# Optimization experiments

Measured on AMD Instinct MI355X. Metric: run time of the kernel, lower is better.

## Reference

```python
import jax, jax.numpy as jnp
import numpy as np

N, NC, D, K = 262144, 4096, 5, 4   # fine dof, coarse dof, nnz/row of A, interp points/row of P
W = 2.0 / 3.0                      # weighted-Jacobi weight
PRE, POST, COARSE = 3, 3, 10       # smoothing counts from the source


def setup_inputs() -> dict:
    key = jax.random.key(0)
    k1, k2, k3, k4, k5 = jax.random.split(key, 5)
    # A in ELL form: slot 0 is the diagonal, made strictly diagonally dominant.
    acols_off = jax.random.randint(k1, (N, D - 1), 0, N)
    A_cols = jnp.concatenate([jnp.arange(N)[:, None], acols_off], axis=1).astype(jnp.int32)
    off = -jax.random.uniform(k2, (N, D - 1), dtype=jnp.float32)          # negative off-diagonals (M-matrix-like)
    diag = 2.0 + jnp.sum(jnp.abs(off), axis=1)
    A_vals = jnp.concatenate([diag[:, None], off], axis=1)
    # P in ELL form: slot 0 maps fine node i -> coarse node i // (N//NC) so every coarse dof is covered.
    pcols_off = jax.random.randint(k3, (N, K - 1), 0, NC)
    P_cols = jnp.concatenate([(jnp.arange(N) // (N // NC))[:, None], pcols_off], axis=1).astype(jnp.int32)
    P_vals = jax.random.uniform(k4, (N, K), dtype=jnp.float32) * 0.5
    b = jax.random.normal(k5, (N,), dtype=jnp.float32)
    x = jnp.zeros((N,), dtype=jnp.float32)
    return {"b": b, "x": x, "A_vals": A_vals, "P_vals": P_vals,
            "A_cols": A_cols, "P_cols": P_cols, "num": 2}


def _spmv(vals, cols, x):
    # ELL SpMV: y[i] = sum_d vals[i,d] * x[cols[i,d]]
    return jnp.sum(vals * x[cols], axis=1)


def _jacobi_ell(vals, cols, diag, b, x, n):
    def step(xc, _):
        return xc + W * (b - _spmv(vals, cols, xc)) / diag, None
    x, _ = jax.lax.scan(step, x, None, length=n)
    return x


def _rap(A_vals, A_cols, P_vals, P_cols):
    # A_c = P^T A P, assembled densely on the coarse level via one big scatter-add.
    Pj_vals = P_vals[A_cols]                                   # [N,D,K]
    Pj_cols = P_cols[A_cols]                                   # [N,D,K]
    vals = (P_vals[:, None, :, None] * A_vals[:, :, None, None]
            * Pj_vals[:, :, None, :])                          # [N,D,K,K]
    a_idx = jnp.broadcast_to(P_cols[:, None, :, None].astype(jnp.int32), (N, D, K, K))
    b_idx = jnp.broadcast_to(Pj_cols[:, :, None, :].astype(jnp.int32), (N, D, K, K))
    flat = (a_idx * NC + b_idx).reshape(-1)
    Ac = jax.ops.segment_sum(vals.reshape(-1), flat, num_segments=NC * NC)
    return Ac.reshape(NC, NC)


def reference(b, x, A_vals, P_vals, A_cols, P_cols, num):
    diag_f = A_vals[:, 0]                      # fine-level diagonal (slot 0)
    Ac = _rap(A_vals, A_cols, P_vals, P_cols)  # coarse operator R A P
    diag_c = jnp.diag(Ac)

    def coarse_solve(bc):
        def step(xc, _):
            return xc + W * (bc - Ac @ xc) / diag_c, None
        xc, _ = jax.lax.scan(step, jnp.zeros((NC,), bc.dtype), None, length=COARSE)
        return xc

    for _ in range(num):                       # mg.Iterate, `num` V-cycles
        x = _jacobi_ell(A_vals, A_cols, diag_f, b, x, PRE)          # pre-smooth
        r = b - _spmv(A_vals, A_cols, x)                            # residual
        bc = jax.ops.segment_sum((P_vals * r[:, None]).reshape(-1),  # restrict: R r = P^T r
                                 P_cols.reshape(-1), num_segments=NC)
        xc = coarse_solve(bc)                                       # coarse Jacobi solve
        x = x + jnp.sum(P_vals * xc[P_cols], axis=1)                # prolongate correction
        x = _jacobi_ell(A_vals, A_cols, diag_f, b, x, POST)         # post-smooth
    return x
```

## Files before the change

### kernel.cpp

```cpp
#include <hip/hip_runtime.h>
#include <hip/hip_fp16.h>

#define NN 262144
#define NCC 4096
#define DD 5
#define PRE_IT 3
#define POST_IT 3
#define COARSE_IT 10
#define WJ ((float)(2.0/3.0))
#define NBLK 256
#define BAR_SLOT_U32 768
#define BAR_SLOTS 40
#define POISON 0xAAAAAAAAu
#define BASE_SUM 0x55555540u

typedef unsigned long long u64;

__device__ __forceinline__ unsigned pack_ch(unsigned col, float v) {
  return col | ((unsigned)__half_as_ushort(__float2half(v)) << 16);
}
__device__ __forceinline__ float unpack_h(unsigned w) {
  return __half2float(__ushort_as_half((unsigned short)(w >> 16)));
}

__device__ __forceinline__ float ldA(const float* p) {
  return __hip_atomic_load(p, __ATOMIC_RELAXED, __HIP_MEMORY_SCOPE_AGENT);
}
__device__ __forceinline__ void stA(float* p, float v) {
  __hip_atomic_store(p, v, __ATOMIC_RELAXED, __HIP_MEMORY_SCOPE_AGENT);
}
__device__ __forceinline__ unsigned ldAu(const unsigned* p) {
  return __hip_atomic_load(p, __ATOMIC_RELAXED, __HIP_MEMORY_SCOPE_AGENT);
}
__device__ __forceinline__ void stAu(unsigned* p, unsigned v) {
  __hip_atomic_store(p, v, __ATOMIC_RELAXED, __HIP_MEMORY_SCOPE_AGENT);
}
__device__ __forceinline__ u64 ldA64(const u64* p) {
  return __hip_atomic_load(p, __ATOMIC_RELAXED, __HIP_MEMORY_SCOPE_AGENT);
}
__device__ __forceinline__ void stA64(u64* p, u64 v) {
  __hip_atomic_store(p, v, __ATOMIC_RELAXED, __HIP_MEMORY_SCOPE_AGENT);
}

__device__ __forceinline__ void gbar(unsigned* bar, int& bs, int* sflag) {
  __syncthreads();
  if (threadIdx.x == 0) {
    unsigned* slot  = bar + bs * BAR_SLOT_U32;
    unsigned* line  = slot + ((blockIdx.x & 31) << 4);
    unsigned* flags = slot + 512;
    unsigned r = __hip_atomic_fetch_add(line, 1u, __ATOMIC_RELAXED,
                                        __HIP_MEMORY_SCOPE_AGENT);
    if ((blockIdx.x & 31) == 0 && r == POISON + 7u) {
      for (;;) {
        unsigned s = 0;
#pragma unroll
        for (int i = 0; i < 32; ++i) s += ldAu(slot + (i << 4));
        if (s - BASE_SUM >= 256u) break;
        __builtin_amdgcn_s_sleep(1);
      }
#pragma unroll
      for (int f = 0; f < 16; ++f) stAu(flags + (f << 4), POISON + 1u);
    }
    const unsigned* fl = flags + ((blockIdx.x & 15) << 4);
    while (ldAu(fl) == POISON) __builtin_amdgcn_s_sleep(1);
    __hip_atomic_store(sflag, bs + 1, __ATOMIC_RELAXED, __HIP_MEMORY_SCOPE_WORKGROUP);
  } else if ((threadIdx.x & 63) == 0) {
    while (__hip_atomic_load(sflag, __ATOMIC_RELAXED, __HIP_MEMORY_SCOPE_WORKGROUP) <= bs)
      __builtin_amdgcn_s_sleep(1);
  }
  ++bs;
}

__global__ __launch_bounds__(1024, 4) void k_all(
    const float* __restrict__ b, const float* __restrict__ x_in,
    const float* __restrict__ A_vals, const float* __restrict__ P_vals,
    const int* __restrict__ A_cols, const int* __restrict__ P_cols,
    const int* __restrict__ num_p,
    unsigned* histG, unsigned* offsG, u64* pairs8,
    unsigned* Y, unsigned* tot,
    unsigned* bar, float* partials, float* x2,
    float* xcA, float* xcB, float* out) {
  extern __shared__ char smem[];
  __shared__ float wdiag[16];
  __shared__ float bcl[16];
  __shared__ unsigned soffs[17];
  __shared__ int sflag;

  const int tid = threadIdx.x;
  const int blk = blockIdx.x;
  const int g = (blk << 10) + tid;
  int bs = 0;
  if (tid == 0) sflag = 0;

  const int4* pc4 = (const int4*)P_cols;
  const float4* pv4 = (const float4*)P_vals;
  unsigned* base_t = histG;

  const int4 pcg = pc4[g];
  const float4 pvg = pv4[g];
  const bool strx = (pcg.x == (g >> 6));
  u64 yreg0, yreg1, yreg2, yreg3, yreg4, yreg5, yreg6, yreg7, yreg8, yreg9;

  {
    unsigned* s1 = (unsigned*)smem;
    unsigned* s2 = s1 + NCC;
    unsigned* s3 = s2 + NCC;
    unsigned* sv = s3 + NCC;

    for (int q = tid; q < NCC; q += 1024) s1[q] = 0u;
    __syncthreads();
    {
      int ac[DD]; float av[DD];
#pragma unroll
      for (int j = 0; j < DD; ++j) { ac[j] = A_cols[g * DD + j]; av[j] = A_vals[g * DD + j]; }
      u64* yp = (u64*)(Y + 20u * (unsigned)g);
      u64 lo_[DD], hi_[DD];
#pragma unroll
      for (int j = 0; j < DD; ++j) {
        const int4 pcn = pc4[ac[j]];
        const float4 pvn = pv4[ac[j]];
        lo_[j] = (u64)pack_ch((unsigned)pcn.x, av[j] * pvn.x)
               | ((u64)pack_ch((unsigned)pcn.y, av[j] * pvn.y) << 32);
        hi_[j] = (u64)pack_ch((unsigned)pcn.z, av[j] * pvn.z)
               | ((u64)pack_ch((unsigned)pcn.w, av[j] * pvn.w) << 32);
        stA64(yp + 2 * j, lo_[j]);
        stA64(yp + 2 * j + 1, hi_[j]);
      }
      yreg0 = lo_[0]; yreg1 = hi_[0]; yreg2 = lo_[1]; yreg3 = hi_[1];
      yreg4 = lo_[2]; yreg5 = hi_[2]; yreg6 = lo_[3]; yreg7 = hi_[3];
      yreg8 = lo_[4]; yreg9 = hi_[4];
    }
    if (!strx) atomicAdd(&s1[pcg.x], 1u);
    atomicAdd(&s1[pcg.y], 1u); atomicAdd(&s1[pcg.z], 1u); atomicAdd(&s1[pcg.w], 1u);
    __syncthreads();
    for (int q = tid; q < NCC; q += 1024) stAu(&histG[(blk << 12) + q], s1[q]);
    gbar(bar, bs, &sflag);

    {
      const int w = tid >> 6, l = tid & 63;
      const int c = (blk << 4) + w;
      const unsigned h0 = ldAu(&histG[(((l << 2) + 0) << 12) + c]);
      const unsigned h1 = ldAu(&histG[(((l << 2) + 1) << 12) + c]);
      const unsigned h2 = ldAu(&histG[(((l << 2) + 2) << 12) + c]);
      const unsigned h3 = ldAu(&histG[(((l << 2) + 3) << 12) + c]);
      const unsigned s = h0 + h1 + h2 + h3;
      unsigned scan = s;
#pragma unroll
      for (int d = 1; d < 64; d <<= 1) {
        unsigned v = __shfl_up(scan, d);
        if (l >= d) scan += v;
      }
      const unsigned pre = scan - s;
      stAu(&base_t[(((l << 2) + 0) << 12) + c], pre);
      stAu(&base_t[(((l << 2) + 1) << 12) + c], pre + h0);
      stAu(&base_t[(((l << 2) + 2) << 12) + c], pre + h0 + h1);
      stAu(&base_t[(((l << 2) + 3) << 12) + c], pre + h0 + h1 + h2);
      if (l == 63) stAu(&tot[c], scan);
    }
    gbar(bar, bs, &sflag);

    {
      for (int q = tid; q < NCC; q += 1024) s1[q] = ldAu(&tot[q]);
      __syncthreads();
      const unsigned a0 = s1[(tid << 2) + 0], a1 = s1[(tid << 2) + 1],
                     a2 = s1[(tid << 2) + 2], a3 = s1[(tid << 2) + 3];
      const unsigned tsum = a0 + a1 + a2 + a3;
      sv[tid] = tsum; __syncthreads();
      for (int off = 1; off < 1024; off <<= 1) {
        unsigned v = (tid >= off) ? sv[tid - off] : 0u;
        __syncthreads();
        sv[tid] += v;
        __syncthreads();
      }
      const unsigned excl = sv[tid] - tsum;
      s1[(tid << 2) + 0] = excl;
      s1[(tid << 2) + 1] = excl + a0;
      s1[(tid << 2) + 2] = excl + a0 + a1;
      s1[(tid << 2) + 3] = excl + a0 + a1 + a2;
      __syncthreads();
      if (tid < 16) stAu(&offsG[(blk << 4) + tid], s1[(blk << 4) + tid]);
      if (blk == 255 && tid == 1023) stAu(&offsG[NCC], excl + tsum);
      for (int q = tid; q < NCC; q += 1024)
        s2[q] = s1[q] + ldAu(&base_t[(blk << 12) + q]);
      for (int q = tid; q < NCC; q += 1024) s3[q] = 0u;
      __syncthreads();
      unsigned r;
      if (!strx) {
        r = atomicAdd(&s3[pcg.x], 1u);
        stA64(&pairs8[s2[pcg.x] + r], (u64)(unsigned)g | ((u64)__float_as_uint(pvg.x) << 32));
      }
      r = atomicAdd(&s3[pcg.y], 1u);
      stA64(&pairs8[s2[pcg.y] + r], (u64)(unsigned)g | ((u64)__float_as_uint(pvg.y) << 32));
      r = atomicAdd(&s3[pcg.z], 1u);
      stA64(&pairs8[s2[pcg.z] + r], (u64)(unsigned)g | ((u64)__float_as_uint(pvg.z) << 32));
      r = atomicAdd(&s3[pcg.w], 1u);
      stA64(&pairs8[s2[pcg.w] + r], (u64)(unsigned)g | ((u64)__float_as_uint(pvg.w) << 32));
    }
    gbar(bar, bs, &sflag);
  }

  __half* slab   = (__half*)smem;
  float* rowbuf  = (float*)(smem + 131072);
  float* rowbuf1 = (float*)(smem + 114688);

  if (tid < 17) soffs[tid] = ldAu(&offsG[(blk << 4) + tid]);

#define SCAT(rb, yk) { \
    const unsigned lo_ = (unsigned)(yk), hi_ = (unsigned)((yk) >> 32); \
    atomicAdd(&rb[lo_ & 0xffffu], pvf * unpack_h(lo_)); \
    atomicAdd(&rb[hi_ & 0xffffu], pvf * unpack_h(hi_)); }
#define SCAT10(rb) { const float pvf = pvg.x; \
    SCAT(rb, yreg0) SCAT(rb, yreg1) SCAT(rb, yreg2) SCAT(rb, yreg3) SCAT(rb, yreg4) \
    SCAT(rb, yreg5) SCAT(rb, yreg6) SCAT(rb, yreg7) SCAT(rb, yreg8) SCAT(rb, yreg9) }

  for (int rp = 0; rp < 8; ++rp) {
    if (rp < 7) {
      const int r0 = rp << 1, r1 = r0 + 1;
      const int c_r0 = (blk << 4) + r0, c_r1 = c_r0 + 1;
      for (int q = tid; q < NCC; q += 1024) { rowbuf[q] = 0.f; rowbuf1[q] = 0.f; }
      __syncthreads();
      const unsigned q0 = soffs[r0], q1 = soffs[r1], q2 = soffs[r1 + 1];
      for (unsigned p = q0 + tid; p < q2; p += 1024) {
        float* rb = (p < q1) ? rowbuf : rowbuf1;
        const u64 e = ldA64(&pairs8[p]);
        const float pvf = __uint_as_float((unsigned)(e >> 32));
        const u64* yp = (const u64*)(Y + 20u * (unsigned)(e & 0xffffffffu));
        u64 y0 = ldA64(yp + 0), y1 = ldA64(yp + 1), y2 = ldA64(yp + 2), y3 = ldA64(yp + 3),
            y4 = ldA64(yp + 4), y5 = ldA64(yp + 5), y6 = ldA64(yp + 6), y7 = ldA64(yp + 7),
            y8 = ldA64(yp + 8), y9 = ldA64(yp + 9);
        SCAT(rb, y0) SCAT(rb, y1) SCAT(rb, y2) SCAT(rb, y3) SCAT(rb, y4)
        SCAT(rb, y5) SCAT(rb, y6) SCAT(rb, y7) SCAT(rb, y8) SCAT(rb, y9)
      }
      if (strx && (pcg.x == c_r0 || pcg.x == c_r1)) {
        float* rb = (pcg.x == c_r0) ? rowbuf : rowbuf1;
        SCAT10(rb)
      }
      __syncthreads();
      if (tid == 0) {
        wdiag[r0] = WJ / rowbuf[(blk << 4) + r0];
        wdiag[r1] = WJ / rowbuf1[(blk << 4) + r1];
      }
      for (int q = tid; q < NCC; q += 1024) {
        slab[(r0 << 12) + q] = __float2half(rowbuf[q]);
        slab[(r1 << 12) + q] = __float2half(rowbuf1[q]);
      }
      __syncthreads();
    } else {
      for (int rr = 14; rr < 16; ++rr) {
        const int c1 = (blk << 4) + rr;
        for (int q = tid; q < NCC; q += 1024) rowbuf[q] = 0.f;
        __syncthreads();
        const unsigned p0 = soffs[rr], p1 = soffs[rr + 1];
        for (unsigned p = p0 + tid; p < p1; p += 1024) {
          const u64 e = ldA64(&pairs8[p]);
          const float pvf = __uint_as_float((unsigned)(e >> 32));
          const u64* yp = (const u64*)(Y + 20u * (unsigned)(e & 0xffffffffu));
          u64 y0 = ldA64(yp + 0), y1 = ldA64(yp + 1), y2 = ldA64(yp + 2), y3 = ldA64(yp + 3),
              y4 = ldA64(yp + 4), y5 = ldA64(yp + 5), y6 = ldA64(yp + 6), y7 = ldA64(yp + 7),
              y8 = ldA64(yp + 8), y9 = ldA64(yp + 9);
          SCAT(rowbuf, y0) SCAT(rowbuf, y1) SCAT(rowbuf, y2) SCAT(rowbuf, y3) SCAT(rowbuf, y4)
          SCAT(rowbuf, y5) SCAT(rowbuf, y6) SCAT(rowbuf, y7) SCAT(rowbuf, y8) SCAT(rowbuf, y9)
        }
        if (strx && pcg.x == c1) { SCAT10(rowbuf) }
        __syncthreads();
        if (tid == 0) wdiag[rr] = WJ / rowbuf[c1];
        for (int q = tid; q < NCC; q += 1024) slab[(rr << 12) + q] = __float2half(rowbuf[q]);
        __syncthreads();
      }
    }
  }
#undef SCAT10
#undef SCAT

  const int num = num_p[0];
  if (num <= 0) { stA(out + g, x_in[g]); return; }

  float av[DD]; int ac[DD];
#pragma unroll
  for (int j = 0; j < DD; ++j) { av[j] = A_vals[g * DD + j]; ac[j] = A_cols[g * DD + j]; }
  const float bg = b[g];
  const float wdg = WJ / av[0];
  float xown = x_in[g];

  const float* xr = x_in;
  int wi = 0;

  for (int cyc = 0; cyc < num; ++cyc) {
    for (int it = 0; it < PRE_IT; ++it) {
      float s = av[0] * xown;
#pragma unroll
      for (int j = 1; j < DD; ++j) s += av[j] * ldA(xr + ac[j]);
      const float xn = xown + (bg - s) * wdg;
      float* wb = (wi == 0) ? x2 : out;
      stA(wb + g, xn);
      xown = xn; xr = wb; wi ^= 1;
      gbar(bar, bs, &sflag);
    }
    {
      float s = av[0] * xown;
#pragma unroll
      for (int j = 1; j < DD; ++j) s += av[j] * ldA(xr + ac[j]);
      const float r = bg - s;
      for (int q = tid; q < NCC; q += 1024) rowbuf[q] = 0.f;
      __syncthreads();
      atomicAdd(&rowbuf[pcg.x], pvg.x * r);
      atomicAdd(&rowbuf[pcg.y], pvg.y * r);
      atomicAdd(&rowbuf[pcg.z], pvg.z * r);
      atomicAdd(&rowbuf[pcg.w], pvg.w * r);
      __syncthreads();
      for (int q = tid; q < NCC; q += 1024) stA(&partials[(blk << 12) + q], rowbuf[q]);
      gbar(bar, bs, &sflag);
    }
    {
      const int t2 = tid >> 2;
      const u64* pp = (const u64*)&partials[(t2 << 12) + (blk << 4)];
      const int qq = (tid & 3) << 1;
      const u64 va = ldA64(pp + qq);
      const u64 vb = ldA64(pp + qq + 1);
      ((u64*)rowbuf)[(t2 << 3) + qq] = va;
      ((u64*)rowbuf)[(t2 << 3) + qq + 1] = vb;
      __syncthreads();
      if (tid < 16) {
        float sum = 0.f;
#pragma unroll 8
        for (int t3 = 0; t3 < 256; ++t3) sum += rowbuf[(t3 << 4) + tid];
        bcl[tid] = sum;
        stA(&xcA[(blk << 4) + tid], sum * wdiag[tid]);
      }
      gbar(bar, bs, &sflag);
    }
    const float* xc_cur = xcA;
    float* xc_nxt = xcB;
    for (int it = 1; it < COARSE_IT; ++it) {
      const u64* xq = (const u64*)(xc_cur + (tid << 2));
      const u64 qa = ldA64(xq), qb = ldA64(xq + 1);
      ((u64*)rowbuf)[(tid << 1)] = qa;
      ((u64*)rowbuf)[(tid << 1) + 1] = qb;
      __syncthreads();
      const int w = tid >> 6, l = tid & 63;
      const __half* srow = slab + (w << 12);
      float acc = 0.f;
#pragma unroll
      for (int k = 0; k < 8; ++k) {
        const int cb = (k << 9) + (l << 3);
        const uint4 hv = *(const uint4*)(srow + cb);
        const float4 x0 = *(const float4*)(rowbuf + cb);
        const float4 x1 = *(const float4*)(rowbuf + cb + 4);
        const float2 h0 = __half22float2(__builtin_bit_cast(__half2, hv.x));
        const float2 h1 = __half22float2(__builtin_bit_cast(__half2, hv.y));
        const float2 h2 = __half22float2(__builtin_bit_cast(__half2, hv.z));
        const float2 h3 = __half22float2(__builtin_bit_cast(__half2, hv.w));
        acc += h0.x * x0.x + h0.y * x0.y + h1.x * x0.z + h1.y * x0.w;
        acc += h2.x * x1.x + h2.y * x1.y + h3.x * x1.z + h3.y * x1.w;
      }
      acc += __shfl_down(acc, 32); acc += __shfl_down(acc, 16);
      acc += __shfl_down(acc, 8);  acc += __shfl_down(acc, 4);
      acc += __shfl_down(acc, 2);  acc += __shfl_down(acc, 1);
      if (l == 0) {
        const float xo = rowbuf[(blk << 4) + w];
        stA(&xc_nxt[(blk << 4) + w], xo + (bcl[w] - acc) * wdiag[w]);
      }
      float* tmp = (float*)xc_cur; xc_cur = xc_nxt; xc_nxt = tmp;
      gbar(bar, bs, &sflag);
    }
    {
      const u64* xq = (const u64*)(xc_cur + (tid << 2));
      const u64 qa = ldA64(xq), qb = ldA64(xq + 1);
      ((u64*)rowbuf)[(tid << 1)] = qa;
      ((u64*)rowbuf)[(tid << 1) + 1] = qb;
      __syncthreads();
      float* xw = (float*)xr;
      const float corr = pvg.x * rowbuf[pcg.x] + pvg.y * rowbuf[pcg.y] +
                         pvg.z * rowbuf[pcg.z] + pvg.w * rowbuf[pcg.w];
      const float xn = xown + corr;
      stA(xw + g, xn);
      xown = xn;
      gbar(bar, bs, &sflag);
    }
    for (int it = 0; it < POST_IT; ++it) {
      float s = av[0] * xown;
#pragma unroll
      for (int j = 1; j < DD; ++j) s += av[j] * ldA(xr + ac[j]);
      const float xn = xown + (bg - s) * wdg;
      float* wb = (wi == 0) ? x2 : out;
      stA(wb + g, xn);
      xown = xn; xr = wb; wi ^= 1;
      if (!(cyc == num - 1 && it == POST_IT - 1)) gbar(bar, bs, &sflag);
    }
  }
}

extern "C" void kernel_launch(void* const* d_in, const int* in_sizes, int n_in,
                              void* d_out, int out_size, void* d_ws, size_t ws_size,
                              hipStream_t stream) {
  (void)in_sizes; (void)n_in; (void)out_size; (void)ws_size;
  const float* b      = (const float*)d_in[0];
  const float* x_in   = (const float*)d_in[1];
  const float* A_vals = (const float*)d_in[2];
  const float* P_vals = (const float*)d_in[3];
  const int*   A_cols = (const int*)d_in[4];
  const int*   P_cols = (const int*)d_in[5];
  const int*   num_p  = (const int*)d_in[6];
  float* out = (float*)d_out;

  char* ws = (char*)d_ws;
  unsigned* offsG  = (unsigned*)(ws + 0);
  unsigned* tot    = (unsigned*)(ws + 20480);
  float*    xcA    = (float*)(ws + 40960);
  float*    xcB    = (float*)(ws + 57344);
  unsigned* bar    = (unsigned*)(ws + 73728);
  u64*      pairs8 = (u64*)(ws + 262144);
  unsigned* histG  = (unsigned*)(ws + 8650752);
  unsigned* Y      = (unsigned*)(ws + 12845056);
  float* partials  = (float*)Y;
  float* x2        = (float*)histG;


  const unsigned smem_bytes = 131072 + 16384;
  hipFuncSetAttribute((const void*)k_all,
                      hipFuncAttributeMaxDynamicSharedMemorySize, (int)smem_bytes);
  hipLaunchKernelGGL(k_all, dim3(NBLK), dim3(1024), smem_bytes, stream,
                     b, x_in, A_vals, P_vals, A_cols, P_cols, num_p,
                     histG, offsG, pairs8, Y, tot,
                     bar, partials, x2, xcA, xcB, out);
}
```

Measured before the change: 475.1 us.

## Give each smoothing step its own fresh buffer so neighbour reads use plain cached loads

For the first two V-cycles, every fine-grid iterate is written to a separate never-before-read buffer, carved out of the reused workspace regions (x2, pairs8, Y). Neighbour gathers can then use ordinary cacheable loads instead of agent-scope atomic loads, since no stale cached copy of that address can exist. The RAP Y-row loads also switch from atomic loads to plain loads. The design depends on workspace aliasing and buffer-lifetime reasoning about stale L2/L1 lines, and it falls back to the old atomic path once the cycle count passes two.

```diff
diff --git a/kernel.cpp b/kernel.cpp
--- a/kernel.cpp
+++ b/kernel.cpp
@@ -40,6 +40,12 @@
 }
 __device__ __forceinline__ void stA64(u64* p, u64 v) {
   __hip_atomic_store(p, v, __ATOMIC_RELAXED, __HIP_MEMORY_SCOPE_AGENT);
+}
+
+__device__ __forceinline__ float* vbuf(float* x2, u64* pairs8, unsigned* Y, int s) {
+  if (s <= 3) return (float*)((char*)x2 + (size_t)s * 1048576u);
+  if (s <= 11) return (float*)((char*)pairs8 + (size_t)(s - 4) * 1048576u);
+  return (float*)((char*)Y + 8388608u);
 }
 
 __device__ __forceinline__ void gbar(unsigned* bar, int& bs, int* sflag) {
@@ -225,9 +231,8 @@
         const u64 e = ldA64(&pairs8[p]);
         const float pvf = __uint_as_float((unsigned)(e >> 32));
         const u64* yp = (const u64*)(Y + 20u * (unsigned)(e & 0xffffffffu));
-        u64 y0 = ldA64(yp + 0), y1 = ldA64(yp + 1), y2 = ldA64(yp + 2), y3 = ldA64(yp + 3),
-            y4 = ldA64(yp + 4), y5 = ldA64(yp + 5), y6 = ldA64(yp + 6), y7 = ldA64(yp + 7),
-            y8 = ldA64(yp + 8), y9 = ldA64(yp + 9);
+        u64 y0 = yp[0], y1 = yp[1], y2 = yp[2], y3 = yp[3], y4 = yp[4],
+            y5 = yp[5], y6 = yp[6], y7 = yp[7], y8 = yp[8], y9 = yp[9];
         SCAT(rb, y0) SCAT(rb, y1) SCAT(rb, y2) SCAT(rb, y3) SCAT(rb, y4)
         SCAT(rb, y5) SCAT(rb, y6) SCAT(rb, y7) SCAT(rb, y8) SCAT(rb, y9)
       }
@@ -255,9 +260,8 @@
           const u64 e = ldA64(&pairs8[p]);
           const float pvf = __uint_as_float((unsigned)(e >> 32));
           const u64* yp = (const u64*)(Y + 20u * (unsigned)(e & 0xffffffffu));
-          u64 y0 = ldA64(yp + 0), y1 = ldA64(yp + 1), y2 = ldA64(yp + 2), y3 = ldA64(yp + 3),
-              y4 = ldA64(yp + 4), y5 = ldA64(yp + 5), y6 = ldA64(yp + 6), y7 = ldA64(yp + 7),
-              y8 = ldA64(yp + 8), y9 = ldA64(yp + 9);
+          u64 y0 = yp[0], y1 = yp[1], y2 = yp[2], y3 = yp[3], y4 = yp[4],
+              y5 = yp[5], y6 = yp[6], y7 = yp[7], y8 = yp[8], y9 = yp[9];
           SCAT(rowbuf, y0) SCAT(rowbuf, y1) SCAT(rowbuf, y2) SCAT(rowbuf, y3) SCAT(rowbuf, y4)
           SCAT(rowbuf, y5) SCAT(rowbuf, y6) SCAT(rowbuf, y7) SCAT(rowbuf, y8) SCAT(rowbuf, y9)
         }
@@ -283,23 +287,32 @@
   float xown = x_in[g];
 
   const float* xr = x_in;
+  bool xr_ag = false;
+  int slot = 0;
   int wi = 0;
 
   for (int cyc = 0; cyc < num; ++cyc) {
+    const bool virg = (cyc < 2);
+    float* const vb1 = vbuf(x2, pairs8, Y, 4);
+    float* const vb2 = vbuf(x2, pairs8, Y, 5);
     for (int it = 0; it < PRE_IT; ++it) {
       float s = av[0] * xown;
 #pragma unroll
-      for (int j = 1; j < DD; ++j) s += av[j] * ldA(xr + ac[j]);
+      for (int j = 1; j < DD; ++j)
+        s += av[j] * ((virg && !xr_ag) ? xr[ac[j]] : ldA(xr + ac[j]));
       const float xn = xown + (bg - s) * wdg;
-      float* wb = (wi == 0) ? x2 : out;
+      float* wb; bool wb_ag;
+      if (virg) { wb = vbuf(x2, pairs8, Y, slot); wb_ag = (slot == 12); ++slot; }
+      else      { wb = (wi == 0) ? vb1 : vb2; wb_ag = true; wi ^= 1; }
       stA(wb + g, xn);
-      xown = xn; xr = wb; wi ^= 1;
+      xown = xn; xr = wb; xr_ag = wb_ag;
       gbar(bar, bs, &sflag);
     }
     {
       float s = av[0] * xown;
 #pragma unroll
-      for (int j = 1; j < DD; ++j) s += av[j] * ldA(xr + ac[j]);
+      for (int j = 1; j < DD; ++j)
+        s += av[j] * ((virg && !xr_ag) ? xr[ac[j]] : ldA(xr + ac[j]));
       const float r = bg - s;
       for (int q = tid; q < NCC; q += 1024) rowbuf[q] = 0.f;
       __syncthreads();
@@ -369,23 +382,30 @@
       ((u64*)rowbuf)[(tid << 1)] = qa;
       ((u64*)rowbuf)[(tid << 1) + 1] = qb;
       __syncthreads();
-      float* xw = (float*)xr;
       const float corr = pvg.x * rowbuf[pcg.x] + pvg.y * rowbuf[pcg.y] +
                          pvg.z * rowbuf[pcg.z] + pvg.w * rowbuf[pcg.w];
       const float xn = xown + corr;
+      float* xw; bool xw_ag;
+      if (virg) { xw = vbuf(x2, pairs8, Y, slot); xw_ag = (slot == 12); ++slot; }
+      else      { xw = (float*)xr; xw_ag = true; }
       stA(xw + g, xn);
-      xown = xn;
+      xown = xn; xr = xw; xr_ag = xw_ag;
       gbar(bar, bs, &sflag);
     }
     for (int it = 0; it < POST_IT; ++it) {
       float s = av[0] * xown;
 #pragma unroll
-      for (int j = 1; j < DD; ++j) s += av[j] * ldA(xr + ac[j]);
+      for (int j = 1; j < DD; ++j)
+        s += av[j] * ((virg && !xr_ag) ? xr[ac[j]] : ldA(xr + ac[j]));
       const float xn = xown + (bg - s) * wdg;
-      float* wb = (wi == 0) ? x2 : out;
+      const bool last = (cyc == num - 1 && it == POST_IT - 1);
+      float* wb; bool wb_ag;
+      if (last)      { wb = out; wb_ag = true; }
+      else if (virg) { wb = vbuf(x2, pairs8, Y, slot); wb_ag = (slot == 12); ++slot; }
+      else           { wb = (wi == 0) ? vb1 : vb2; wb_ag = true; wi ^= 1; }
       stA(wb + g, xn);
-      xown = xn; xr = wb; wi ^= 1;
-      if (!(cyc == num - 1 && it == POST_IT - 1)) gbar(bar, bs, &sflag);
+      xown = xn; xr = wb; xr_ag = wb_ag;
+      if (!last) gbar(bar, bs, &sflag);
     }
   }
 }
```

After: 460.9 us. -3.0%, faster.
